# Kernel tuning notes

Measured on AMD Instinct MI355X. Metric: run time of the kernel, lower is better.

The kernel has to match this reference:

```python
import jax, jax.numpy as jnp
import numpy as np

B, S, D, H = 1, 4096, 1024, 16
HD = D // H  # 64

def _precompute_freqs_cis(dim, end, theta=10000.0):
    freqs = 1.0 / theta ** (jnp.arange(0, dim, 2, dtype=jnp.float32) / dim)
    t = jnp.arange(end, dtype=jnp.float32)
    freqs = jnp.outer(t, freqs)
    return jnp.cos(freqs), jnp.sin(freqs)

def setup_inputs() -> dict:
    key = jax.random.key(0)
    ks = jax.random.split(key, 5)
    cos, sin = _precompute_freqs_cis(HD, S)
    scale = 1.0 / np.sqrt(D)
    return {
        "hidden_states": jax.random.normal(ks[0], (B, S, D), dtype=jnp.float32),
        "cos": cos,
        "sin": sin,
        "attention_mask": jnp.ones((B, S), dtype=jnp.float32),
        "Wq": jax.random.normal(ks[1], (D, D), dtype=jnp.float32) * scale,
        "Wk": jax.random.normal(ks[2], (D, D), dtype=jnp.float32) * scale,
        "Wv": jax.random.normal(ks[3], (D, D), dtype=jnp.float32) * scale,
        "Wo": jax.random.normal(ks[4], (D, D), dtype=jnp.float32) * scale,
    }

def _rope(x, cos, sin):
    # x: [B,S,H,HD]; cos/sin: [S,HD//2] -> broadcast [1,S,1,HD//2]
    c = cos[None, :, None, :]
    s = sin[None, :, None, :]
    x1, x2 = jnp.split(x, 2, axis=-1)
    return jnp.concatenate([x1 * c - x2 * s, x2 * c + x1 * s], axis=-1)

def reference(hidden_states, cos, sin, attention_mask, Wq, Wk, Wv, Wo):
    b, s, d = hidden_states.shape
    h, hd = H, HD
    q = (hidden_states @ Wq.T).reshape(b, s, h, hd)
    k = (hidden_states @ Wk.T).reshape(b, s, h, hd)
    v = (hidden_states @ Wv.T).reshape(b, s, h, hd)
    q = _rope(q, cos, sin)
    k = _rope(k, cos, sin)
    scaling = hd ** (-0.5)
    # [B,H,S,S] scores (naive full-matrix attention, matching source)
    scores = jnp.einsum('bqhd,bkhd->bhqk', q, k) * scaling
    mask_add = (1.0 - attention_mask)[:, None, None, :] * (-10000.0)
    scores = scores + mask_add
    attn = jax.nn.softmax(scores.astype(jnp.float32), axis=-1).astype(q.dtype)
    out = jnp.einsum('bhqk,bkhd->bqhd', attn, v).reshape(b, s, d)
    return out @ Wo.T
```

## Files before the change

kernel.cpp:

```cpp
#include <hip/hip_runtime.h>
#include <stdint.h>

#define S_LEN   4096
#define D_MODEL 1024
#define N_HEADS 16
#define HEAD_DIM 64
#define LDP 72

typedef __attribute__((ext_vector_type(8))) short bf16x8;
typedef __attribute__((ext_vector_type(4))) float f32x4;
typedef __attribute__((ext_vector_type(4))) unsigned short u16x4;
typedef unsigned short ushort_t;

#define LOG2E 1.44269504088896340736f
#define FIX_MAX 20.0f

__device__ __forceinline__ ushort_t f2bf(float f) {
    union { float f; uint32_t u; } v; v.f = f;
    uint32_t u = v.u;
    return (ushort_t)((u + 0x7fffu + ((u >> 16) & 1u)) >> 16);
}
__device__ __forceinline__ ushort_t f2bf_fast(float f) {
    union { float f; uint32_t u; } v; v.f = f;
    return (ushort_t)((v.u + 0x8000u) >> 16);
}
__device__ __forceinline__ float ex2(float x) {
#if __has_builtin(__builtin_amdgcn_exp2f)
    return __builtin_amdgcn_exp2f(x);
#else
    return exp2f(x);
#endif
}
__device__ __forceinline__ bf16x8 cvt8(const float* __restrict__ p) {
    bf16x8 r;
#pragma unroll
    for (int j = 0; j < 8; j++) r[j] = (short)f2bf(p[j]);
    return r;
}
__device__ __forceinline__ void gl_lds16(const ushort_t* g, ushort_t* l) {
    __builtin_amdgcn_global_load_lds(
        (const __attribute__((address_space(1))) void*)g,
        (__attribute__((address_space(3))) void*)l,
        16, 0, 0);
}

__global__ __launch_bounds__(256)
void cvtall_kernel(const float* __restrict__ X,  const float* __restrict__ Wq,
                   const float* __restrict__ Wk, const float* __restrict__ Wv,
                   const float* __restrict__ Wo, const float* __restrict__ mask,
                   ushort_t* __restrict__ Xb,  ushort_t* __restrict__ Wqb,
                   ushort_t* __restrict__ Wkb, ushort_t* __restrict__ Wvb,
                   ushort_t* __restrict__ Wob, float* __restrict__ maddArr)
{
    int b = blockIdx.x;
    if (b < 4096) {
        const float* src; ushort_t* dst; size_t off;
        if (b < 2048)      { src = X;  dst = Xb;  off = (size_t)b * 2048; }
        else if (b < 2560) { src = Wq; dst = Wqb; off = (size_t)(b - 2048) * 2048; }
        else if (b < 3072) { src = Wk; dst = Wkb; off = (size_t)(b - 2560) * 2048; }
        else if (b < 3584) { src = Wv; dst = Wvb; off = (size_t)(b - 3072) * 2048; }
        else               { src = Wo; dst = Wob; off = (size_t)(b - 3584) * 2048; }
        size_t i = off + (size_t)threadIdx.x * 8;
        *(bf16x8*)(dst + i) = cvt8(src + i);
    } else {
        int i = (b - 4096) * 256 + threadIdx.x;
        maddArr[i] = fmaf(1.0f - mask[i], -10000.0f * LOG2E, -FIX_MAX);
    }
}

__global__ __launch_bounds__(256)
void madd_kernel(const float* __restrict__ mask, float* __restrict__ maddArr)
{
    int i = blockIdx.x * 256 + threadIdx.x;
    if (i < S_LEN)
        maddArr[i] = fmaf(1.0f - mask[i], -10000.0f * LOG2E, -FIX_MAX);
}

template <int ASYNC>
__global__ __launch_bounds__(256)
void qkv_kernel(const float* __restrict__ Xf, const ushort_t* __restrict__ Xb,
                const float* __restrict__ Wqf, const float* __restrict__ Wkf, const float* __restrict__ Wvf,
                const ushort_t* __restrict__ Wqb, const ushort_t* __restrict__ Wkb, const ushort_t* __restrict__ Wvb,
                ushort_t* __restrict__ Qo, ushort_t* __restrict__ Ko, ushort_t* __restrict__ Vto,
                const float* __restrict__ cosF, const float* __restrict__ sinF)
{
    __shared__ __align__(16) ushort_t As[128 * 64];
    __shared__ __align__(16) ushort_t Bs[128 * 64];

    const int t     = threadIdx.x;
    const int mode  = blockIdx.x >> 3;
    const int mBase = blockIdx.y * 128;
    const int nBase = (blockIdx.x & 7) * 128;
    const int lane  = t & 63;
    const int wid   = t >> 6;
    const int quad  = lane >> 4;
    const int l15   = lane & 15;
    const int sw    = l15 & 7;
    const int wm    = (wid & 1) * 64;
    const int wn    = (wid >> 1) * 64;

    const float*    Wf = (mode == 0) ? Wqf : (mode == 1) ? Wkf : Wvf;
    const ushort_t* Wb = (mode == 0) ? Wqb : (mode == 1) ? Wkb : Wvb;

    f32x4 acc[4][4];
#pragma unroll
    for (int i = 0; i < 4; i++)
#pragma unroll
        for (int j = 0; j < 4; j++) acc[i][j] = (f32x4)(0.0f);

    for (int k0 = 0; k0 < D_MODEL; k0 += 64) {
#pragma unroll
        for (int i = 0; i < 4; i++) {
            int e   = (i * 256 + t) * 8;
            int row = e >> 6;
            int c   = ((e >> 3) & 7) ^ (row & 7);
            if (ASYNC) {
                gl_lds16(&Xb[(size_t)(mBase + row) * D_MODEL + k0 + c * 8], &As[e]);
                gl_lds16(&Wb[(size_t)(nBase + row) * D_MODEL + k0 + c * 8], &Bs[e]);
            } else {
                *(bf16x8*)(&As[e]) = cvt8(&Xf[(size_t)(mBase + row) * D_MODEL + k0 + c * 8]);
                *(bf16x8*)(&Bs[e]) = cvt8(&Wf[(size_t)(nBase + row) * D_MODEL + k0 + c * 8]);
            }
        }
        __syncthreads();
#pragma unroll
        for (int ks = 0; ks < 2; ks++) {
            bf16x8 a[4], b[4];
            const int cc = ((ks * 4 + quad) ^ sw) * 8;
#pragma unroll
            for (int mt = 0; mt < 4; mt++)
                a[mt] = *(const bf16x8*)(&As[((wm + mt * 16 + l15) << 6) + cc]);
#pragma unroll
            for (int nt = 0; nt < 4; nt++)
                b[nt] = *(const bf16x8*)(&Bs[((wn + nt * 16 + l15) << 6) + cc]);
#pragma unroll
            for (int mt = 0; mt < 4; mt++)
#pragma unroll
                for (int nt = 0; nt < 4; nt++)
                    acc[mt][nt] = __builtin_amdgcn_mfma_f32_16x16x32_bf16(a[mt], b[nt], acc[mt][nt], 0, 0, 0);
        }
        __syncthreads();
    }

    if (mode == 2) {
#pragma unroll
        for (int mt = 0; mt < 4; mt++) {
            int m0 = mBase + wm + mt * 16 + quad * 4;
#pragma unroll
            for (int nt = 0; nt < 4; nt++) {
                int n = nBase + wn + nt * 16 + l15;
                u16x4 pk;
#pragma unroll
                for (int r = 0; r < 4; r++) pk[r] = f2bf(acc[mt][nt][r]);
                *(u16x4*)(&Vto[(size_t)n * S_LEN + m0]) = pk;
            }
        }
    } else {
        ushort_t* outB = (mode == 0) ? Qo : Ko;
        const float sc = (mode == 0) ? (0.125f * LOG2E) : 1.0f;
        const int hcb = nBase + wn;
#pragma unroll
        for (int nt = 0; nt < 2; nt++) {
            int f = nt * 16 + l15;
#pragma unroll
            for (int mt = 0; mt < 4; mt++) {
                int m0 = mBase + wm + mt * 16 + quad * 4;
#pragma unroll
                for (int r = 0; r < 4; r++) {
                    int srow = m0 + r;
                    float c = cosF[srow * 32 + f];
                    float s = sinF[srow * 32 + f];
                    float x1 = acc[mt][nt][r];
                    float x2 = acc[mt][nt + 2][r];
                    outB[(size_t)srow * D_MODEL + hcb + f]      = f2bf((x1 * c - x2 * s) * sc);
                    outB[(size_t)srow * D_MODEL + hcb + 32 + f] = f2bf((x2 * c + x1 * s) * sc);
                }
            }
        }
    }
}

template <int ASYNC>
__global__ __launch_bounds__(256)
void oproj_kernel(const ushort_t* __restrict__ Ab,
                  const float* __restrict__ Wf, const ushort_t* __restrict__ Wb,
                  float* __restrict__ outF)
{
    __shared__ __align__(16) ushort_t As[64 * 64];
    __shared__ __align__(16) ushort_t Bs[128 * 64];

    const int t     = threadIdx.x;
    const int mBase = blockIdx.y * 64;
    const int nBase = blockIdx.x * 128;
    const int lane  = t & 63;
    const int wid   = t >> 6;
    const int quad  = lane >> 4;
    const int l15   = lane & 15;
    const int sw    = l15 & 7;
    const int wm    = (wid & 1) * 32;
    const int wn    = (wid >> 1) * 64;

    f32x4 acc[2][4];
#pragma unroll
    for (int i = 0; i < 2; i++)
#pragma unroll
        for (int j = 0; j < 4; j++) acc[i][j] = (f32x4)(0.0f);

    for (int k0 = 0; k0 < D_MODEL; k0 += 64) {
#pragma unroll
        for (int i = 0; i < 2; i++) {
            int e = (i * 256 + t) * 8;
            int row = e >> 6;
            int c = ((e >> 3) & 7) ^ (row & 7);
            gl_lds16(&Ab[(size_t)(mBase + row) * D_MODEL + k0 + c * 8], &As[e]);
        }
#pragma unroll
        for (int i = 0; i < 4; i++) {
            int e = (i * 256 + t) * 8;
            int row = e >> 6;
            int c = ((e >> 3) & 7) ^ (row & 7);
            if (ASYNC) gl_lds16(&Wb[(size_t)(nBase + row) * D_MODEL + k0 + c * 8], &Bs[e]);
            else       *(bf16x8*)(&Bs[e]) = cvt8(&Wf[(size_t)(nBase + row) * D_MODEL + k0 + c * 8]);
        }
        __syncthreads();
#pragma unroll
        for (int ks = 0; ks < 2; ks++) {
            bf16x8 a[2], b[4];
            const int cc = ((ks * 4 + quad) ^ sw) * 8;
#pragma unroll
            for (int mt = 0; mt < 2; mt++)
                a[mt] = *(const bf16x8*)(&As[((wm + mt * 16 + l15) << 6) + cc]);
#pragma unroll
            for (int nt = 0; nt < 4; nt++)
                b[nt] = *(const bf16x8*)(&Bs[((wn + nt * 16 + l15) << 6) + cc]);
#pragma unroll
            for (int mt = 0; mt < 2; mt++)
#pragma unroll
                for (int nt = 0; nt < 4; nt++)
                    acc[mt][nt] = __builtin_amdgcn_mfma_f32_16x16x32_bf16(a[mt], b[nt], acc[mt][nt], 0, 0, 0);
        }
        __syncthreads();
    }

#pragma unroll
    for (int mt = 0; mt < 2; mt++) {
        int m0 = mBase + wm + mt * 16 + quad * 4;
#pragma unroll
        for (int nt = 0; nt < 4; nt++) {
            int n = nBase + wn + nt * 16 + l15;
#pragma unroll
            for (int r = 0; r < 4; r++)
                outF[(size_t)(m0 + r) * D_MODEL + n] = acc[mt][nt][r];
        }
    }
}

__global__ __launch_bounds__(256)
void attn_kernel(const ushort_t* __restrict__ Q, const ushort_t* __restrict__ K,
                 const ushort_t* __restrict__ Vt, const float* __restrict__ maddArr,
                 ushort_t* __restrict__ out)
{
    __shared__ __align__(16) ushort_t Ks[2][64 * 64];
    __shared__ __align__(16) ushort_t Vs[2][64 * 64];
    __shared__ __align__(16) ushort_t Ps[128 * LDP];

    const int t    = threadIdx.x;
    const int h    = blockIdx.y;
    const int qt   = blockIdx.x;
    const int lane = t & 63;
    const int wid  = t >> 6;
    const int quad = lane >> 4;
    const int l15  = lane & 15;
    const int sw   = l15 & 7;
    const int wq   = wid * 32;

    bf16x8 aq[2][2];
#pragma unroll
    for (int mt = 0; mt < 2; mt++)
#pragma unroll
        for (int ks = 0; ks < 2; ks++)
            aq[mt][ks] = *(const bf16x8*)(&Q[(size_t)(qt * 128 + wq + mt * 16 + l15) * D_MODEL
                                            + h * HEAD_DIM + ks * 32 + quad * 8]);

    bf16x8 ones;
#pragma unroll
    for (int j = 0; j < 8; j++) ones[j] = (short)0x3F80;

    const int e0 = t * 8,   e1 = (256 + t) * 8;
    const int r0 = e0 >> 6, r1 = e1 >> 6;
    const int c0 = ((e0 >> 3) & 7) ^ (r0 & 7);
    const int c1 = ((e1 >> 3) & 7) ^ (r1 & 7);
    const ushort_t* kS0 = K  + (size_t)r0 * D_MODEL + h * HEAD_DIM + c0 * 8;
    const ushort_t* kS1 = K  + (size_t)r1 * D_MODEL + h * HEAD_DIM + c1 * 8;
    const ushort_t* vS0 = Vt + (size_t)(h * HEAD_DIM + r0) * S_LEN + c0 * 8;
    const ushort_t* vS1 = Vt + (size_t)(h * HEAD_DIM + r1) * S_LEN + c1 * 8;
    const float*    mP  = maddArr + l15;

    f32x4 o_acc[2][4];
    f32x4 l_frag[2];
#pragma unroll
    for (int mt = 0; mt < 2; mt++) {
        l_frag[mt] = (f32x4)(0.0f);
#pragma unroll
        for (int nt = 0; nt < 4; nt++) o_acc[mt][nt] = (f32x4)(0.0f);
    }

    gl_lds16(kS0, &Ks[0][e0]);
    gl_lds16(kS1, &Ks[0][e1]);
    gl_lds16(vS0, &Vs[0][e0]);
    gl_lds16(vS1, &Vs[0][e1]);
    kS0 += 64 * D_MODEL; kS1 += 64 * D_MODEL; vS0 += 64; vS1 += 64;

    for (int kt = 0; kt < S_LEN / 64; kt++) {
        const int cur = kt & 1, nxt = cur ^ 1;
        __syncthreads();

        float ma0 = mP[0], ma1 = mP[16], ma2 = mP[32], ma3 = mP[48];
        mP += 64;

        if (kt < S_LEN / 64 - 1) {
            gl_lds16(kS0, &Ks[nxt][e0]);
            gl_lds16(kS1, &Ks[nxt][e1]);
            gl_lds16(vS0, &Vs[nxt][e0]);
            gl_lds16(vS1, &Vs[nxt][e1]);
        }
        kS0 += 64 * D_MODEL; kS1 += 64 * D_MODEL; vS0 += 64; vS1 += 64;

        f32x4 sacc[2][4];
#pragma unroll
        for (int mt = 0; mt < 2; mt++) {
            sacc[mt][0] = (f32x4)(ma0);
            sacc[mt][1] = (f32x4)(ma1);
            sacc[mt][2] = (f32x4)(ma2);
            sacc[mt][3] = (f32x4)(ma3);
        }
#pragma unroll
        for (int ks = 0; ks < 2; ks++) {
            bf16x8 bk[4];
            const int cc = ((ks * 4 + quad) ^ sw) * 8;
#pragma unroll
            for (int nt = 0; nt < 4; nt++)
                bk[nt] = *(const bf16x8*)(&Ks[cur][((nt * 16 + l15) << 6) + cc]);
#pragma unroll
            for (int mt = 0; mt < 2; mt++)
#pragma unroll
                for (int nt = 0; nt < 4; nt++)
                    sacc[mt][nt] = __builtin_amdgcn_mfma_f32_16x16x32_bf16(aq[mt][ks], bk[nt], sacc[mt][nt], 0, 0, 0);
        }

#pragma unroll
        for (int mt = 0; mt < 2; mt++) {
            ushort_t* psw = &Ps[(wq + mt * 16 + quad * 4) * LDP + l15];
#pragma unroll
            for (int r = 0; r < 4; r++) {
                psw[r * LDP]      = f2bf_fast(ex2(fminf(sacc[mt][0][r], 0.0f)));
                psw[r * LDP + 16] = f2bf_fast(ex2(fminf(sacc[mt][1][r], 0.0f)));
                psw[r * LDP + 32] = f2bf_fast(ex2(fminf(sacc[mt][2][r], 0.0f)));
                psw[r * LDP + 48] = f2bf_fast(ex2(fminf(sacc[mt][3][r], 0.0f)));
            }
        }

#pragma unroll
        for (int ks = 0; ks < 2; ks++) {
            bf16x8 ap[2], bv[4];
#pragma unroll
            for (int mt = 0; mt < 2; mt++)
                ap[mt] = *(const bf16x8*)(&Ps[(wq + mt * 16 + l15) * LDP + ks * 32 + quad * 8]);
            const int cc = ((ks * 4 + quad) ^ sw) * 8;
#pragma unroll
            for (int nt = 0; nt < 4; nt++)
                bv[nt] = *(const bf16x8*)(&Vs[cur][((nt * 16 + l15) << 6) + cc]);
#pragma unroll
            for (int mt = 0; mt < 2; mt++) {
#pragma unroll
                for (int nt = 0; nt < 4; nt++)
                    o_acc[mt][nt] = __builtin_amdgcn_mfma_f32_16x16x32_bf16(ap[mt], bv[nt], o_acc[mt][nt], 0, 0, 0);
                l_frag[mt] = __builtin_amdgcn_mfma_f32_16x16x32_bf16(ap[mt], ones, l_frag[mt], 0, 0, 0);
            }
        }
    }

#pragma unroll
    for (int mt = 0; mt < 2; mt++) {
#pragma unroll
        for (int r = 0; r < 4; r++) {
            float inv = 1.0f / fmaxf(l_frag[mt][r], 1e-30f);
            int srow = qt * 128 + wq + mt * 16 + quad * 4 + r;
#pragma unroll
            for (int nt = 0; nt < 4; nt++) {
                int col = h * HEAD_DIM + nt * 16 + l15;
                out[(size_t)srow * D_MODEL + col] = f2bf(o_acc[mt][nt][r] * inv);
            }
        }
    }
}

extern "C" void kernel_launch(void* const* d_in, const int* in_sizes, int n_in,
                              void* d_out, int out_size, void* d_ws, size_t ws_size,
                              hipStream_t stream)
{
    (void)in_sizes; (void)n_in; (void)out_size;

    const float* X    = (const float*)d_in[0];
    const float* cosF = (const float*)d_in[1];
    const float* sinF = (const float*)d_in[2];
    const float* mask = (const float*)d_in[3];
    const float* Wq   = (const float*)d_in[4];
    const float* Wk   = (const float*)d_in[5];
    const float* Wv   = (const float*)d_in[6];
    const float* Wo   = (const float*)d_in[7];

    const size_t SD = (size_t)S_LEN * D_MODEL;
    const size_t WD = (size_t)D_MODEL * D_MODEL;
    ushort_t* ws  = (ushort_t*)d_ws;
    ushort_t* Qb  = ws;
    ushort_t* Kb  = ws + SD;
    ushort_t* Vtb = ws + 2 * SD;
    ushort_t* Ab  = ws + 3 * SD;
    float* outF   = (float*)d_out;
    float* maddArr = outF;

    dim3 gQKV(24, 32), gO(8, 64), gA(S_LEN / 128, N_HEADS), bb(256);
    const bool big = ws_size >= (size_t)40 * 1024 * 1024;

    if (big) {
        ushort_t* Xb  = Ab;
        ushort_t* Wqb = ws + 4 * SD;
        ushort_t* Wkb = Wqb + WD;
        ushort_t* Wvb = Wkb + WD;
        ushort_t* Wob = Wvb + WD;

        cvtall_kernel<<<4112, 256, 0, stream>>>(X, Wq, Wk, Wv, Wo, mask,
                                                Xb, Wqb, Wkb, Wvb, Wob, maddArr);
        qkv_kernel<1><<<gQKV, bb, 0, stream>>>(nullptr, Xb, nullptr, nullptr, nullptr,
                                               Wqb, Wkb, Wvb, Qb, Kb, Vtb, cosF, sinF);
        attn_kernel<<<gA, bb, 0, stream>>>(Qb, Kb, Vtb, maddArr, Ab);
        oproj_kernel<1><<<gO, bb, 0, stream>>>(Ab, nullptr, Wob, outF);
    } else {
        madd_kernel<<<S_LEN / 256, 256, 0, stream>>>(mask, maddArr);
        qkv_kernel<0><<<gQKV, bb, 0, stream>>>(X, nullptr, Wq, Wk, Wv,
                                               nullptr, nullptr, nullptr, Qb, Kb, Vtb, cosF, sinF);
        attn_kernel<<<gA, bb, 0, stream>>>(Qb, Kb, Vtb, maddArr, Ab);
        oproj_kernel<0><<<gO, bb, 0, stream>>>(Ab, Wo, nullptr, outF);
    }
}
```

Measured before the change: 286.8 us.

## Permute key order to vectorize P stores and stage bf16 inputs in output buffer

```diff
diff --git a/kernel.cpp b/kernel.cpp
--- a/kernel.cpp
+++ b/kernel.cpp
@@ -47,40 +47,30 @@
 __global__ __launch_bounds__(256)
 void cvtall_kernel(const float* __restrict__ X,  const float* __restrict__ Wq,
                    const float* __restrict__ Wk, const float* __restrict__ Wv,
-                   const float* __restrict__ Wo, const float* __restrict__ mask,
+                   const float* __restrict__ mask,
                    ushort_t* __restrict__ Xb,  ushort_t* __restrict__ Wqb,
                    ushort_t* __restrict__ Wkb, ushort_t* __restrict__ Wvb,
-                   ushort_t* __restrict__ Wob, float* __restrict__ maddArr)
+                   float* __restrict__ maddArr)
 {
     int b = blockIdx.x;
-    if (b < 4096) {
+    if (b < 3584) {
         const float* src; ushort_t* dst; size_t off;
         if (b < 2048)      { src = X;  dst = Xb;  off = (size_t)b * 2048; }
         else if (b < 2560) { src = Wq; dst = Wqb; off = (size_t)(b - 2048) * 2048; }
         else if (b < 3072) { src = Wk; dst = Wkb; off = (size_t)(b - 2560) * 2048; }
-        else if (b < 3584) { src = Wv; dst = Wvb; off = (size_t)(b - 3072) * 2048; }
-        else               { src = Wo; dst = Wob; off = (size_t)(b - 3584) * 2048; }
+        else               { src = Wv; dst = Wvb; off = (size_t)(b - 3072) * 2048; }
         size_t i = off + (size_t)threadIdx.x * 8;
         *(bf16x8*)(dst + i) = cvt8(src + i);
     } else {
-        int i = (b - 4096) * 256 + threadIdx.x;
+        int i = (b - 3584) * 256 + threadIdx.x;
         maddArr[i] = fmaf(1.0f - mask[i], -10000.0f * LOG2E, -FIX_MAX);
     }
 }
 
 __global__ __launch_bounds__(256)
-void madd_kernel(const float* __restrict__ mask, float* __restrict__ maddArr)
-{
-    int i = blockIdx.x * 256 + threadIdx.x;
-    if (i < S_LEN)
-        maddArr[i] = fmaf(1.0f - mask[i], -10000.0f * LOG2E, -FIX_MAX);
-}
-
-template <int ASYNC>
-__global__ __launch_bounds__(256)
-void qkv_kernel(const float* __restrict__ Xf, const ushort_t* __restrict__ Xb,
-                const float* __restrict__ Wqf, const float* __restrict__ Wkf, const float* __restrict__ Wvf,
-                const ushort_t* __restrict__ Wqb, const ushort_t* __restrict__ Wkb, const ushort_t* __restrict__ Wvb,
+void qkv_kernel(const ushort_t* __restrict__ Xb,
+                const ushort_t* __restrict__ Wqb, const ushort_t* __restrict__ Wkb,
+                const ushort_t* __restrict__ Wvb,
                 ushort_t* __restrict__ Qo, ushort_t* __restrict__ Ko, ushort_t* __restrict__ Vto,
                 const float* __restrict__ cosF, const float* __restrict__ sinF)
 {
@@ -99,7 +89,6 @@
     const int wm    = (wid & 1) * 64;
     const int wn    = (wid >> 1) * 64;
 
-    const float*    Wf = (mode == 0) ? Wqf : (mode == 1) ? Wkf : Wvf;
     const ushort_t* Wb = (mode == 0) ? Wqb : (mode == 1) ? Wkb : Wvb;
 
     f32x4 acc[4][4];
@@ -114,13 +103,8 @@
             int e   = (i * 256 + t) * 8;
             int row = e >> 6;
             int c   = ((e >> 3) & 7) ^ (row & 7);
-            if (ASYNC) {
-                gl_lds16(&Xb[(size_t)(mBase + row) * D_MODEL + k0 + c * 8], &As[e]);
-                gl_lds16(&Wb[(size_t)(nBase + row) * D_MODEL + k0 + c * 8], &Bs[e]);
-            } else {
-                *(bf16x8*)(&As[e]) = cvt8(&Xf[(size_t)(mBase + row) * D_MODEL + k0 + c * 8]);
-                *(bf16x8*)(&Bs[e]) = cvt8(&Wf[(size_t)(nBase + row) * D_MODEL + k0 + c * 8]);
-            }
+            gl_lds16(&Xb[(size_t)(mBase + row) * D_MODEL + k0 + c * 8], &As[e]);
+            gl_lds16(&Wb[(size_t)(nBase + row) * D_MODEL + k0 + c * 8], &Bs[e]);
         }
         __syncthreads();
 #pragma unroll
@@ -143,16 +127,16 @@
     }
 
     if (mode == 2) {
+        const int sbase = mBase + wm;
 #pragma unroll
         for (int mt = 0; mt < 4; mt++) {
-            int m0 = mBase + wm + mt * 16 + quad * 4;
 #pragma unroll
             for (int nt = 0; nt < 4; nt++) {
                 int n = nBase + wn + nt * 16 + l15;
-                u16x4 pk;
-#pragma unroll
-                for (int r = 0; r < 4; r++) pk[r] = f2bf(acc[mt][nt][r]);
-                *(u16x4*)(&Vto[(size_t)n * S_LEN + m0]) = pk;
+#pragma unroll
+                for (int r = 0; r < 4; r++)
+                    Vto[(size_t)n * S_LEN + sbase + ((quad * 4 + r) << 2) + mt] =
+                        f2bf(acc[mt][nt][r]);
             }
         }
     } else {
@@ -180,10 +164,8 @@
     }
 }
 
-template <int ASYNC>
 __global__ __launch_bounds__(256)
-void oproj_kernel(const ushort_t* __restrict__ Ab,
-                  const float* __restrict__ Wf, const ushort_t* __restrict__ Wb,
+void oproj_kernel(const ushort_t* __restrict__ Ab, const float* __restrict__ Wf,
                   float* __restrict__ outF)
 {
     __shared__ __align__(16) ushort_t As[64 * 64];
@@ -219,8 +201,7 @@
             int e = (i * 256 + t) * 8;
             int row = e >> 6;
             int c = ((e >> 3) & 7) ^ (row & 7);
-            if (ASYNC) gl_lds16(&Wb[(size_t)(nBase + row) * D_MODEL + k0 + c * 8], &Bs[e]);
-            else       *(bf16x8*)(&Bs[e]) = cvt8(&Wf[(size_t)(nBase + row) * D_MODEL + k0 + c * 8]);
+            *(bf16x8*)(&Bs[e]) = cvt8(&Wf[(size_t)(nBase + row) * D_MODEL + k0 + c * 8]);
         }
         __syncthreads();
 #pragma unroll
@@ -296,6 +277,9 @@
     const ushort_t* vS1 = Vt + (size_t)(h * HEAD_DIM + r1) * S_LEN + c1 * 8;
     const float*    mP  = maddArr + l15;
 
+    ushort_t* psw0 = &Ps[(wq + quad * 4) * LDP + (l15 << 2)];
+    ushort_t* psw1 = &Ps[(wq + 16 + quad * 4) * LDP + (l15 << 2)];
+
     f32x4 o_acc[2][4];
     f32x4 l_frag[2];
 #pragma unroll
@@ -350,13 +334,15 @@
 
 #pragma unroll
         for (int mt = 0; mt < 2; mt++) {
-            ushort_t* psw = &Ps[(wq + mt * 16 + quad * 4) * LDP + l15];
+            ushort_t* psw = mt ? psw1 : psw0;
 #pragma unroll
             for (int r = 0; r < 4; r++) {
-                psw[r * LDP]      = f2bf_fast(ex2(fminf(sacc[mt][0][r], 0.0f)));
-                psw[r * LDP + 16] = f2bf_fast(ex2(fminf(sacc[mt][1][r], 0.0f)));
-                psw[r * LDP + 32] = f2bf_fast(ex2(fminf(sacc[mt][2][r], 0.0f)));
-                psw[r * LDP + 48] = f2bf_fast(ex2(fminf(sacc[mt][3][r], 0.0f)));
+                u16x4 pk;
+                pk[0] = f2bf_fast(ex2(fminf(sacc[mt][0][r], 0.0f)));
+                pk[1] = f2bf_fast(ex2(fminf(sacc[mt][1][r], 0.0f)));
+                pk[2] = f2bf_fast(ex2(fminf(sacc[mt][2][r], 0.0f)));
+                pk[3] = f2bf_fast(ex2(fminf(sacc[mt][3][r], 0.0f)));
+                *(u16x4*)(&psw[r * LDP]) = pk;
             }
         }
 
@@ -399,7 +385,7 @@
                               void* d_out, int out_size, void* d_ws, size_t ws_size,
                               hipStream_t stream)
 {
-    (void)in_sizes; (void)n_in; (void)out_size;
+    (void)in_sizes; (void)n_in; (void)out_size; (void)ws_size;
 
     const float* X    = (const float*)d_in[0];
     const float* cosF = (const float*)d_in[1];
@@ -412,35 +398,26 @@
 
     const size_t SD = (size_t)S_LEN * D_MODEL;
     const size_t WD = (size_t)D_MODEL * D_MODEL;
+
     ushort_t* ws  = (ushort_t*)d_ws;
     ushort_t* Qb  = ws;
     ushort_t* Kb  = ws + SD;
     ushort_t* Vtb = ws + 2 * SD;
     ushort_t* Ab  = ws + 3 * SD;
-    float* outF   = (float*)d_out;
-    float* maddArr = outF;
+
+    float*    outF    = (float*)d_out;
+    float*    maddArr = outF;
+    ushort_t* ob      = (ushort_t*)d_out;
+    ushort_t* Xb      = ob + 8192;
+    ushort_t* Wqb     = Xb + SD;
+    ushort_t* Wkb     = Wqb + WD;
+    ushort_t* Wvb     = Wkb + WD;
 
     dim3 gQKV(24, 32), gO(8, 64), gA(S_LEN / 128, N_HEADS), bb(256);
-    const bool big = ws_size >= (size_t)40 * 1024 * 1024;
-
-    if (big) {
-        ushort_t* Xb  = Ab;
-        ushort_t* Wqb = ws + 4 * SD;
-        ushort_t* Wkb = Wqb + WD;
-        ushort_t* Wvb = Wkb + WD;
-        ushort_t* Wob = Wvb + WD;
-
-        cvtall_kernel<<<4112, 256, 0, stream>>>(X, Wq, Wk, Wv, Wo, mask,
-                                                Xb, Wqb, Wkb, Wvb, Wob, maddArr);
-        qkv_kernel<1><<<gQKV, bb, 0, stream>>>(nullptr, Xb, nullptr, nullptr, nullptr,
-                                               Wqb, Wkb, Wvb, Qb, Kb, Vtb, cosF, sinF);
-        attn_kernel<<<gA, bb, 0, stream>>>(Qb, Kb, Vtb, maddArr, Ab);
-        oproj_kernel<1><<<gO, bb, 0, stream>>>(Ab, nullptr, Wob, outF);
-    } else {
-        madd_kernel<<<S_LEN / 256, 256, 0, stream>>>(mask, maddArr);
-        qkv_kernel<0><<<gQKV, bb, 0, stream>>>(X, nullptr, Wq, Wk, Wv,
-                                               nullptr, nullptr, nullptr, Qb, Kb, Vtb, cosF, sinF);
-        attn_kernel<<<gA, bb, 0, stream>>>(Qb, Kb, Vtb, maddArr, Ab);
-        oproj_kernel<0><<<gO, bb, 0, stream>>>(Ab, Wo, nullptr, outF);
-    }
-}
+
+    cvtall_kernel<<<3600, bb, 0, stream>>>(X, Wq, Wk, Wv, mask,
+                                           Xb, Wqb, Wkb, Wvb, maddArr);
+    qkv_kernel<<<gQKV, bb, 0, stream>>>(Xb, Wqb, Wkb, Wvb, Qb, Kb, Vtb, cosF, sinF);
+    attn_kernel<<<gA, bb, 0, stream>>>(Qb, Kb, Vtb, maddArr, Ab);
+    oproj_kernel<<<gO, bb, 0, stream>>>(Ab, Wo, outF);
+}
```

After: 297.7 us. 1.04x slower.
